# Performance work log

Hardware: AMD Instinct MI355X
Metric: run time of the kernel (lower is better)

Reference implementation:

```python
import jax, jax.numpy as jnp
import numpy as np

N = 100_000          # nodes
E = 1_600_000        # random edges (self-loops added inside gat_conv, as PyG does)
F_IN = 14
DIM = 8
HEADS = 8
NEG_SLOPE = 0.2      # PyG GATConv default negative_slope


def _gat_conv(x, edge_index, W, a_src, a_dst, bias, heads, dim, concat):
    """Faithful PyG GATConv (eval mode): self-loops, per-head linear,
    leaky-relu attention logits, segment softmax over dst, scatter-add."""
    n = x.shape[0]
    loop = jnp.arange(n)
    src = jnp.concatenate([edge_index[0], loop])   # source j
    dst = jnp.concatenate([edge_index[1], loop])   # target i (aggregation index)

    h = (x @ W).reshape(n, heads, dim)             # [N, H, D]
    alpha_src = jnp.einsum('nhd,hd->nh', h, a_src)  # [N, H]
    alpha_dst = jnp.einsum('nhd,hd->nh', h, a_dst)

    e = jax.nn.leaky_relu(alpha_src[src] + alpha_dst[dst], NEG_SLOPE)  # [E', H]
    # segment softmax over incoming edges of each dst node
    m = jax.ops.segment_max(e, dst, num_segments=n)                     # [N, H]
    ex = jnp.exp(e - m[dst])
    s = jax.ops.segment_sum(ex, dst, num_segments=n)
    alpha = ex / (s[dst] + 1e-16)                                       # [E', H]

    msg = h[src] * alpha[:, :, None]                                    # [E', H, D]
    out = jax.ops.segment_sum(msg, dst, num_segments=n)                 # [N, H, D]
    out = out.reshape(n, heads * dim) if concat else out.mean(axis=1)
    return out + bias


def setup_inputs() -> dict:
    key = jax.random.key(0)
    ks = jax.random.split(key, 10)
    x = jax.random.normal(ks[0], (N, F_IN), jnp.float32)
    edge_index = jax.random.randint(ks[1], (2, E), 0, N, dtype=jnp.int64)
    W1 = jax.random.normal(ks[2], (F_IN, HEADS * DIM), jnp.float32) * 0.3
    att_src1 = jax.random.normal(ks[3], (HEADS, DIM), jnp.float32) * 0.3
    att_dst1 = jax.random.normal(ks[4], (HEADS, DIM), jnp.float32) * 0.3
    bias1 = jnp.zeros((HEADS * DIM,), jnp.float32)
    W2 = jax.random.normal(ks[5], (HEADS * DIM, DIM), jnp.float32) * 0.15
    att_src2 = jax.random.normal(ks[6], (1, DIM), jnp.float32) * 0.3
    att_dst2 = jax.random.normal(ks[7], (1, DIM), jnp.float32) * 0.3
    bias2 = jnp.zeros((DIM,), jnp.float32)
    return {"x": x, "edge_index": edge_index,
            "W1": W1, "att_src1": att_src1, "att_dst1": att_dst1, "bias1": bias1,
            "W2": W2, "att_src2": att_src2, "att_dst2": att_dst2, "bias2": bias2}


def reference(x, edge_index, W1, att_src1, att_dst1, bias1,
              W2, att_src2, att_dst2, bias2):
    # dropout layers are identity in eval mode
    h = jax.nn.elu(_gat_conv(x, edge_index, W1, att_src1, att_dst1, bias1,
                             HEADS, DIM, concat=True))      # [N, 64]
    out = _gat_conv(h, edge_index, W2, att_src2, att_dst2, bias2,
                    1, DIM, concat=False)                   # [N, 8]
    return out
```

## Files before the change

### kernel.cpp

```cpp
#include <hip/hip_runtime.h>
#include <math.h>

#define F_IN 14
#define NSLOPE 0.2f
#define BSHIFT 7
#define BSZ 128
#define CAP 4096
#define NBMAX 1024
#define PAD 32
#define CHUNK 8192

typedef __attribute__((ext_vector_type(8))) unsigned short u16x8;

__device__ __forceinline__ float leaky(float v) { return v >= 0.f ? v : NSLOPE * v; }

__device__ __forceinline__ float b2f(unsigned short u) {
    union { float f; unsigned int i; } v; v.i = ((unsigned int)u) << 16; return v.f;
}
__device__ __forceinline__ unsigned short f2b(float f) {
    union { float f; unsigned int i; } v; v.f = f;
    unsigned int r = v.i + 0x7FFFu + ((v.i >> 16) & 1u);
    return (unsigned short)(r >> 16);
}


__global__ void init_cur(int* __restrict__ cur_p, int NB) {
    int i = blockIdx.x * blockDim.x + threadIdx.x;
    if (i < NB) cur_p[i * PAD] = i * CAP;
}

__global__ __launch_bounds__(512)
void k_scatter_k1(const int* __restrict__ ei, int E,
                  int* __restrict__ cur_p, int* __restrict__ stage, int NB,
                  int nchunk,
                  const float* __restrict__ x,
                  const float* __restrict__ W1,
                  const float* __restrict__ a_src,
                  const float* __restrict__ a_dst,
                  unsigned short* __restrict__ h1b,
                  unsigned short* __restrict__ as1b,
                  float* __restrict__ ad1,
                  int N)
{
    __shared__ int hist[NBMAX];
    __shared__ int wbase[NBMAX];
    __shared__ float W[F_IN * 64];
    int t = threadIdx.x;
    if (blockIdx.x < (unsigned)nchunk) {
        for (int b = t; b < NB; b += 512) hist[b] = 0;
        __syncthreads();
        int base = blockIdx.x * CHUNK;
        int end = min(base + CHUNK, E);
        for (int k = base + t; k < end; k += 512)
            atomicAdd(&hist[ei[E + k] >> BSHIFT], 1);
        __syncthreads();
        for (int b = t; b < NB; b += 512) {
            int c = hist[b];
            wbase[b] = c ? atomicAdd(&cur_p[b * PAD], c) : 0;
            hist[b] = 0;
        }
        __syncthreads();
        for (int k = base + t; k < end; k += 512) {
            int j = ei[k];
            int i = ei[E + k];
            int key = i >> BSHIFT;
            int ofs = atomicAdd(&hist[key], 1);
            int pos = wbase[key] + ofs;
            if (pos < (key + 1) * CAP)
                stage[pos] = j | ((i & (BSZ - 1)) << 17);
        }
    } else {
        for (int idx = t; idx < F_IN * 64; idx += 512) W[idx] = W1[idx];
        __syncthreads();
        int node = (blockIdx.x - nchunk) * 8 + (t >> 6);
        int f = t & 63;
        if (node >= N) return;
        const float* xr = x + (size_t)node * F_IN;
        float h = 0.f;
#pragma unroll
        for (int k = 0; k < F_IN; ++k) h += xr[k] * W[k * 64 + f];
        int head = f >> 3, d = f & 7;
        float vs = h * a_src[head * 8 + d];
        float vd = h * a_dst[head * 8 + d];
        vs += __shfl_xor(vs, 1, 8); vs += __shfl_xor(vs, 2, 8); vs += __shfl_xor(vs, 4, 8);
        vd += __shfl_xor(vd, 1, 8); vd += __shfl_xor(vd, 2, 8); vd += __shfl_xor(vd, 4, 8);
        if (d == 0) {
            as1b[node * 8 + head] = f2b(vs);
            ad1[node * 8 + head] = vd;
        }
        h1b[(size_t)node * 64 + f] = f2b(h);
    }
}

__global__ void pass2(const int* __restrict__ cur_p,
                      const int* __restrict__ stage,
                      int* __restrict__ rowstart, int* __restrict__ deg,
                      int* __restrict__ csr, int N) {
    int b = blockIdx.x;
    int node0 = b << BSHIFT;
    int nn = min(BSZ, N - node0);
    int base = b * CAP;
    int cnt = min(cur_p[b * PAD] - base, CAP);
    __shared__ int hist[BSZ];
    __shared__ int excl[BSZ];
    __shared__ int cur[BSZ];
    __shared__ int recs[CAP];
    int t = threadIdx.x;
    if (t < BSZ) hist[t] = 0;
    __syncthreads();
    const int* sp = stage + base;
    for (int k = t; k < cnt; k += 256) {
        int r = sp[k];
        recs[k] = r;
        atomicAdd(&hist[r >> 17], 1);
    }
    __syncthreads();
    if (t < BSZ) excl[t] = hist[t];
    __syncthreads();
    for (int off = 1; off < BSZ; off <<= 1) {
        int v = (t < BSZ && t >= off) ? excl[t - off] : 0;
        __syncthreads();
        if (t < BSZ) excl[t] += v;
        __syncthreads();
    }
    if (t < BSZ) excl[t] -= hist[t];
    __syncthreads();
    if (t < nn) {
        rowstart[node0 + t] = base + excl[t];
        deg[node0 + t] = hist[t];
        cur[t] = base + excl[t];
    }
    __syncthreads();
    for (int k = t; k < cnt; k += 256) {
        int r = recs[k];
        int pos = atomicAdd(&cur[r >> 17], 1);
        csr[pos] = r & 0x1FFFF;
    }
}


__global__ void k2_fused(const int* __restrict__ rowstart,
                         const int* __restrict__ deg,
                         const int* __restrict__ csr,
                         const unsigned short* __restrict__ h1b,
                         const unsigned short* __restrict__ as1b,
                         const float* __restrict__ ad1,
                         const float* __restrict__ bias1,
                         const float* __restrict__ W2,
                         const float* __restrict__ asw2,
                         const float* __restrict__ adw2,
                         float* __restrict__ h2,
                         float* __restrict__ as2,
                         float* __restrict__ ad2, int N)
{
    int t = threadIdx.x;
    int node = blockIdx.x * 32 + (t >> 3);
    int head = t & 7;
    if (node >= N) return;
    float adi = ad1[node * 8 + head];
    float asi = b2f(as1b[node * 8 + head]);
    float ex = __expf(leaky(asi + adi));
    float den = ex;
    u16x8 a = *(const u16x8*)(h1b + (size_t)node * 64 + head * 8);
    float n[8];
#pragma unroll
    for (int u = 0; u < 8; ++u) n[u] = ex * b2f(a[u]);
    int base = rowstart[node], cnt = deg[node];
    int k = 0;
    for (; k + 4 <= cnt; k += 4) {
        int j0 = csr[base + k];
        int j1 = csr[base + k + 1];
        int j2 = csr[base + k + 2];
        int j3 = csr[base + k + 3];
        float e0 = __expf(leaky(b2f(as1b[j0 * 8 + head]) + adi));
        float e1 = __expf(leaky(b2f(as1b[j1 * 8 + head]) + adi));
        float e2 = __expf(leaky(b2f(as1b[j2 * 8 + head]) + adi));
        float e3 = __expf(leaky(b2f(as1b[j3 * 8 + head]) + adi));
        u16x8 r0 = *(const u16x8*)(h1b + (size_t)j0 * 64 + head * 8);
        u16x8 r1 = *(const u16x8*)(h1b + (size_t)j1 * 64 + head * 8);
        u16x8 r2 = *(const u16x8*)(h1b + (size_t)j2 * 64 + head * 8);
        u16x8 r3 = *(const u16x8*)(h1b + (size_t)j3 * 64 + head * 8);
        den += (e0 + e1) + (e2 + e3);
#pragma unroll
        for (int u = 0; u < 8; ++u)
            n[u] += (e0 * b2f(r0[u]) + e1 * b2f(r1[u])) + (e2 * b2f(r2[u]) + e3 * b2f(r3[u]));
    }
    for (; k < cnt; ++k) {
        int j0 = csr[base + k];
        float e0 = __expf(leaky(b2f(as1b[j0 * 8 + head]) + adi));
        u16x8 r0 = *(const u16x8*)(h1b + (size_t)j0 * 64 + head * 8);
        den += e0;
#pragma unroll
        for (int u = 0; u < 8; ++u) n[u] += e0 * b2f(r0[u]);
    }
    float inv = 1.f / (den + 1e-16f);
    float v[8];
    const float* bp = bias1 + head * 8;
#pragma unroll
    for (int u = 0; u < 8; ++u) {
        float w = n[u] * inv + bp[u];
        v[u] = w > 0.f ? w : (__expf(w) - 1.f);
    }
    float p[8];
    const float* wrow = W2 + head * 64;
#pragma unroll
    for (int o = 0; o < 8; ++o) {
        float s = 0.f;
#pragma unroll
        for (int u = 0; u < 8; ++u) s += v[u] * wrow[u * 8 + o];
        p[o] = s;
    }
#pragma unroll
    for (int o = 0; o < 8; ++o) {
        p[o] += __shfl_xor(p[o], 1, 8);
        p[o] += __shfl_xor(p[o], 2, 8);
        p[o] += __shfl_xor(p[o], 4, 8);
    }
    float vs = 0.f, vd = 0.f;
#pragma unroll
    for (int o = 0; o < 8; ++o) { vs += p[o] * asw2[o]; vd += p[o] * adw2[o]; }
    if (head == 0) { as2[node] = vs; ad2[node] = vd; }
    float hv = p[0];
#pragma unroll
    for (int o = 1; o < 8; ++o) hv = (head == o) ? p[o] : hv;
    h2[(size_t)node * 8 + head] = hv;
}


__global__ void k4_gather_l2(const int* __restrict__ rowstart,
                             const int* __restrict__ deg,
                             const int* __restrict__ csr,
                             const float* __restrict__ h2,
                             const float* __restrict__ as2,
                             const float* __restrict__ ad2,
                             const float* __restrict__ bias2,
                             float* __restrict__ out, int N)
{
    int t = threadIdx.x;
    int node = blockIdx.x * 32 + (t >> 3);
    int d = t & 7;
    if (node >= N) return;
    float adi = ad2[node];
    float ex = __expf(leaky(as2[node] + adi));
    float den = ex;
    float num = ex * h2[(size_t)node * 8 + d];
    int base = rowstart[node], cnt = deg[node];
    int k = 0;
    for (; k + 8 <= cnt; k += 8) {
        int j0 = csr[base + k];
        int j1 = csr[base + k + 1];
        int j2 = csr[base + k + 2];
        int j3 = csr[base + k + 3];
        int j4 = csr[base + k + 4];
        int j5 = csr[base + k + 5];
        int j6 = csr[base + k + 6];
        int j7 = csr[base + k + 7];
        float e0 = __expf(leaky(as2[j0] + adi));
        float e1 = __expf(leaky(as2[j1] + adi));
        float e2 = __expf(leaky(as2[j2] + adi));
        float e3 = __expf(leaky(as2[j3] + adi));
        float e4 = __expf(leaky(as2[j4] + adi));
        float e5 = __expf(leaky(as2[j5] + adi));
        float e6 = __expf(leaky(as2[j6] + adi));
        float e7 = __expf(leaky(as2[j7] + adi));
        float v0 = h2[(size_t)j0 * 8 + d];
        float v1 = h2[(size_t)j1 * 8 + d];
        float v2 = h2[(size_t)j2 * 8 + d];
        float v3 = h2[(size_t)j3 * 8 + d];
        float v4 = h2[(size_t)j4 * 8 + d];
        float v5 = h2[(size_t)j5 * 8 + d];
        float v6 = h2[(size_t)j6 * 8 + d];
        float v7 = h2[(size_t)j7 * 8 + d];
        den += ((e0 + e1) + (e2 + e3)) + ((e4 + e5) + (e6 + e7));
        num += ((e0 * v0 + e1 * v1) + (e2 * v2 + e3 * v3))
             + ((e4 * v4 + e5 * v5) + (e6 * v6 + e7 * v7));
    }
    for (; k + 4 <= cnt; k += 4) {
        int j0 = csr[base + k];
        int j1 = csr[base + k + 1];
        int j2 = csr[base + k + 2];
        int j3 = csr[base + k + 3];
        float e0 = __expf(leaky(as2[j0] + adi));
        float e1 = __expf(leaky(as2[j1] + adi));
        float e2 = __expf(leaky(as2[j2] + adi));
        float e3 = __expf(leaky(as2[j3] + adi));
        float v0 = h2[(size_t)j0 * 8 + d];
        float v1 = h2[(size_t)j1 * 8 + d];
        float v2 = h2[(size_t)j2 * 8 + d];
        float v3 = h2[(size_t)j3 * 8 + d];
        den += (e0 + e1) + (e2 + e3);
        num += (e0 * v0 + e1 * v1) + (e2 * v2 + e3 * v3);
    }
    for (; k < cnt; ++k) {
        int j0 = csr[base + k];
        float e0 = __expf(leaky(as2[j0] + adi));
        den += e0;
        num += e0 * h2[(size_t)j0 * 8 + d];
    }
    out[(size_t)node * 8 + d] = num / (den + 1e-16f) + bias2[d];
}


extern "C" void kernel_launch(void* const* d_in, const int* in_sizes, int n_in,
                              void* d_out, int out_size, void* d_ws, size_t ws_size,
                              hipStream_t stream) {
    const float* x    = (const float*)d_in[0];
    const int*   ei   = (const int*)d_in[1];
    const float* W1   = (const float*)d_in[2];
    const float* asw1 = (const float*)d_in[3];
    const float* adw1 = (const float*)d_in[4];
    const float* b1   = (const float*)d_in[5];
    const float* W2   = (const float*)d_in[6];
    const float* asw2 = (const float*)d_in[7];
    const float* adw2 = (const float*)d_in[8];
    const float* b2   = (const float*)d_in[9];
    float* out = (float*)d_out;

    int N = in_sizes[0] / F_IN;
    int E = in_sizes[1] / 2;
    int NB = (N + BSZ - 1) >> BSHIFT;
    int nchunk = (E + CHUNK - 1) / CHUNK;
    int k1blk = (N + 7) / 8;

    float* fw  = (float*)d_ws;
    float* h2  = fw;
    float* as2 = h2  + (size_t)N * 8;
    float* ad2 = as2 + (size_t)N;
    float* ad1 = ad2 + (size_t)N;
    unsigned short* h1b  = (unsigned short*)(ad1 + (size_t)N * 8);
    unsigned short* as1b = h1b + (size_t)N * 64;
    int* deg      = (int*)(as1b + (size_t)N * 8);
    int* rowstart = deg + N;
    int* cur_p    = rowstart + N;
    int* csr      = cur_p + NBMAX * PAD;
    int* stage    = csr + (size_t)NB * CAP;

    init_cur<<<(NB + 255) / 256, 256, 0, stream>>>(cur_p, NB);
    k_scatter_k1<<<nchunk + k1blk, 512, 0, stream>>>(ei, E, cur_p, stage, NB, nchunk,
                                                     x, W1, asw1, adw1, h1b, as1b, ad1, N);
    pass2<<<NB, 256, 0, stream>>>(cur_p, stage, rowstart, deg, csr, N);

    k2_fused<<<(N + 31) / 32, 256, 0, stream>>>(rowstart, deg, csr, h1b, as1b, ad1,
                                                b1, W2, asw2, adw2, h2, as2, ad2, N);

    k4_gather_l2<<<(N + 31) / 32, 256, 0, stream>>>(rowstart, deg, csr, h2, as2, ad2, b2, out, N);
}
```

Baseline: 136.0 us.

## Sort edges per chunk in LDS and build bucket offsets from per-chunk table

Each scatter block now sorts its chunk of edges by destination bucket in shared memory, using a local prefix scan. It writes the sorted chunk to the staging buffer with coalesced vector stores and records per-bucket offsets in a per-chunk table. This replaces the global atomic cursor allocation and the separate init kernel. Pass2 scans the per-chunk segment lengths and uses a binary search to gather each bucket's records from many small segments. The trade-offs are fragmented, less coalesced reads in pass2 and more shared memory in the fused scatter/linear kernel.

```diff
diff --git a/kernel.cpp b/kernel.cpp
--- a/kernel.cpp
+++ b/kernel.cpp
@@ -7,7 +7,7 @@
 #define BSZ 128
 #define CAP 4096
 #define NBMAX 1024
-#define PAD 32
+#define NCHUNKMAX 256
 #define CHUNK 8192
 
 typedef __attribute__((ext_vector_type(8))) unsigned short u16x8;
@@ -24,14 +24,9 @@
 }
 
 
-__global__ void init_cur(int* __restrict__ cur_p, int NB) {
-    int i = blockIdx.x * blockDim.x + threadIdx.x;
-    if (i < NB) cur_p[i * PAD] = i * CAP;
-}
-
 __global__ __launch_bounds__(512)
 void k_scatter_k1(const int* __restrict__ ei, int E,
-                  int* __restrict__ cur_p, int* __restrict__ stage, int NB,
+                  int* __restrict__ stage, int* __restrict__ tab, int NB,
                   int nchunk,
                   const float* __restrict__ x,
                   const float* __restrict__ W1,
@@ -43,32 +38,49 @@
                   int N)
 {
     __shared__ int hist[NBMAX];
-    __shared__ int wbase[NBMAX];
+    __shared__ int s0[NBMAX];
+    __shared__ int cur[NBMAX];
+    __shared__ int srt[CHUNK];
     __shared__ float W[F_IN * 64];
     int t = threadIdx.x;
     if (blockIdx.x < (unsigned)nchunk) {
-        for (int b = t; b < NB; b += 512) hist[b] = 0;
-        __syncthreads();
         int base = blockIdx.x * CHUNK;
         int end = min(base + CHUNK, E);
+        int cnt = end - base;
+        for (int b = t; b < NBMAX; b += 512) hist[b] = 0;
+        __syncthreads();
         for (int k = base + t; k < end; k += 512)
             atomicAdd(&hist[ei[E + k] >> BSHIFT], 1);
         __syncthreads();
-        for (int b = t; b < NB; b += 512) {
-            int c = hist[b];
-            wbase[b] = c ? atomicAdd(&cur_p[b * PAD], c) : 0;
-            hist[b] = 0;
-        }
+        s0[t] = hist[t];
+        s0[t + 512] = hist[t + 512];
+        __syncthreads();
+        for (int off = 1; off < NBMAX; off <<= 1) {
+            int v1 = (t >= off) ? s0[t - off] : 0;
+            int v2 = (t + 512 >= off) ? s0[t + 512 - off] : 0;
+            __syncthreads();
+            s0[t] += v1;
+            s0[t + 512] += v2;
+            __syncthreads();
+        }
+        cur[t] = s0[t] - hist[t];
+        cur[t + 512] = s0[t + 512] - hist[t + 512];
         __syncthreads();
         for (int k = base + t; k < end; k += 512) {
             int j = ei[k];
             int i = ei[E + k];
             int key = i >> BSHIFT;
-            int ofs = atomicAdd(&hist[key], 1);
-            int pos = wbase[key] + ofs;
-            if (pos < (key + 1) * CAP)
-                stage[pos] = j | ((i & (BSZ - 1)) << 17);
-        }
+            int pos = atomicAdd(&cur[key], 1);
+            srt[pos] = j | ((i & (BSZ - 1)) << 17);
+        }
+        __syncthreads();
+        for (int k = t * 4; k < cnt; k += 2048) {
+            int4 v = *(const int4*)&srt[k];
+            *(int4*)&stage[base + k] = v;
+        }
+        int* tr = tab + (size_t)blockIdx.x * (NBMAX + 1);
+        for (int b = t; b < NB; b += 512) tr[b] = s0[b] - hist[b];
+        if (t == 0) tr[NB] = cnt;
     } else {
         for (int idx = t; idx < F_IN * 64; idx += 512) W[idx] = W1[idx];
         __syncthreads();
@@ -92,25 +104,49 @@
     }
 }
 
-__global__ void pass2(const int* __restrict__ cur_p,
-                      const int* __restrict__ stage,
-                      int* __restrict__ rowstart, int* __restrict__ deg,
-                      int* __restrict__ csr, int N) {
+
+__global__ __launch_bounds__(256)
+void pass2(const int* __restrict__ stage, const int* __restrict__ tab, int nchunk,
+           int* __restrict__ rowstart, int* __restrict__ deg,
+           int* __restrict__ csr, int N) {
     int b = blockIdx.x;
     int node0 = b << BSHIFT;
     int nn = min(BSZ, N - node0);
     int base = b * CAP;
-    int cnt = min(cur_p[b * PAD] - base, CAP);
+    __shared__ int segstart[NCHUNKMAX];
+    __shared__ int cum[NCHUNKMAX];
     __shared__ int hist[BSZ];
     __shared__ int excl[BSZ];
     __shared__ int cur[BSZ];
     __shared__ int recs[CAP];
     int t = threadIdx.x;
+    {
+        int len = 0, s = 0;
+        if (t < nchunk) {
+            const int* tr = tab + (size_t)t * (NBMAX + 1);
+            s = tr[b];
+            len = tr[b + 1] - s;
+        }
+        segstart[t] = s;
+        cum[t] = len;
+    }
     if (t < BSZ) hist[t] = 0;
     __syncthreads();
-    const int* sp = stage + base;
+    for (int off = 1; off < NCHUNKMAX; off <<= 1) {
+        int v = (t >= off) ? cum[t - off] : 0;
+        __syncthreads();
+        cum[t] += v;
+        __syncthreads();
+    }
+    int cnt = min(cum[NCHUNKMAX - 1], CAP);
     for (int k = t; k < cnt; k += 256) {
-        int r = sp[k];
+        int lo = 0, hi = NCHUNKMAX - 1;
+        while (lo < hi) {
+            int mid = (lo + hi) >> 1;
+            if (cum[mid] > k) hi = mid; else lo = mid + 1;
+        }
+        int prev = lo ? cum[lo - 1] : 0;
+        int r = stage[lo * CHUNK + segstart[lo] + (k - prev)];
         recs[k] = r;
         atomicAdd(&hist[r >> 17], 1);
     }
@@ -331,14 +367,13 @@
     unsigned short* as1b = h1b + (size_t)N * 64;
     int* deg      = (int*)(as1b + (size_t)N * 8);
     int* rowstart = deg + N;
-    int* cur_p    = rowstart + N;
-    int* csr      = cur_p + NBMAX * PAD;
+    int* csr      = rowstart + N;
     int* stage    = csr + (size_t)NB * CAP;
-
-    init_cur<<<(NB + 255) / 256, 256, 0, stream>>>(cur_p, NB);
-    k_scatter_k1<<<nchunk + k1blk, 512, 0, stream>>>(ei, E, cur_p, stage, NB, nchunk,
+    int* tab      = stage + (size_t)nchunk * CHUNK;
+
+    k_scatter_k1<<<nchunk + k1blk, 512, 0, stream>>>(ei, E, stage, tab, NB, nchunk,
                                                      x, W1, asw1, adw1, h1b, as1b, ad1, N);
-    pass2<<<NB, 256, 0, stream>>>(cur_p, stage, rowstart, deg, csr, N);
+    pass2<<<NB, 256, 0, stream>>>(stage, tab, nchunk, rowstart, deg, csr, N);
 
     k2_fused<<<(N + 31) / 32, 256, 0, stream>>>(rowstart, deg, csr, h1b, as1b, ad1,
                                                 b1, W2, asw2, adw2, h2, as2, ad2, N);
```

New measurement: 131.7 us. -3.2%, faster.
